# Optimization experiments

Measured on AMD Instinct MI355X. Metric: run time of the kernel, lower is better.

The kernel has to match this reference:

```python
import jax, jax.numpy as jnp
import numpy as np

N_NODES = 100000

def gcn_conv(x, W, b, src, dst, n):
    # PyG GCNConv: h = x @ W; add self-loops; norm = D^-1/2 (A+I) D^-1/2; aggregate at dst.
    h = x @ W  # [N, out]
    deg = jnp.zeros((n,), h.dtype).at[dst].add(1.0) + 1.0  # +1 for self-loop
    d = jax.lax.rsqrt(deg)  # deg >= 1 always
    norm = d[src] * d[dst]  # [E]
    agg = jnp.zeros_like(h).at[dst].add(norm[:, None] * h[src])  # scatter-add neighbor messages
    agg = agg + h * (d * d)[:, None]  # self-loop contribution (norm = d_i^2)
    return agg + b


def setup_inputs() -> dict:
    key = jax.random.key(0)
    k1, k2, k3, k4 = jax.random.split(key, 4)
    F_in, H, C = 128, 64, 16
    E = 3200000
    x = jax.random.normal(k1, (N_NODES, F_in), dtype=jnp.float32)
    edges = jax.random.randint(k2, (E, 2), 0, N_NODES, dtype=jnp.int64)
    # Glorot-style init for weights, zero bias (as in GCNConv.reset_parameters)
    W1 = jax.random.normal(k3, (F_in, H), dtype=jnp.float32) * (1.0 / np.sqrt(F_in))
    b1 = jnp.zeros((H,), jnp.float32)
    W2 = jax.random.normal(k4, (H, C), dtype=jnp.float32) * (1.0 / np.sqrt(H))
    b2 = jnp.zeros((C,), jnp.float32)
    return {"x": x, "edges": edges, "W1": W1, "b1": b1, "W2": W2, "b2": b2}


def reference(x, edges, W1, b1, W2, b2):
    src, dst = edges[:, 0], edges[:, 1]
    h = jax.nn.relu(gcn_conv(x, W1, b1, src, dst, N_NODES))
    out = gcn_conv(h, W2, b2, src, dst, N_NODES)
    return out
```

## Files before the change

kernel.cpp:

```cpp
#include <hip/hip_runtime.h>

#define N_NODES 100000
#define F_IN    128
#define H_DIM   64
#define C_DIM   16
#define NBKT    391
#define CHUNK   8192
#define CAP     8960
#define MAXCH   400

typedef __attribute__((ext_vector_type(8))) short bf16x8;
typedef __attribute__((ext_vector_type(4))) float f32x4;

__device__ __forceinline__ unsigned bfr(float f) {
    unsigned u = __float_as_uint(f);
    return (u + (((u >> 16) & 1u) + 0x7FFFu)) >> 16;
}
__device__ __forceinline__ void accb(float4& a, uint2 u) {
    a.x += __uint_as_float(u.x << 16);
    a.y += __uint_as_float(u.x & 0xFFFF0000u);
    a.z += __uint_as_float(u.y << 16);
    a.w += __uint_as_float(u.y & 0xFFFF0000u);
}

__global__ __launch_bounds__(512) void k_bfill(const int2* __restrict__ edges,
                                               int* __restrict__ pairs_flat,
                                               int* __restrict__ cnts_g,
                                               int* __restrict__ lbase_g, int E) {
    __shared__ int2 sp[CHUNK];
    __shared__ int  cnt[NBKT];
    __shared__ int  lbase[NBKT];
    __shared__ int  scn[512];
    int t = threadIdx.x;
    for (int i = t; i < NBKT; i += 512) cnt[i] = 0;
    __syncthreads();
    int base = blockIdx.x * CHUNK;
    int m    = min(E - base, CHUNK);
    int2 ed[16];
    int  rk[16];
    #pragma unroll
    for (int i = 0; i < 16; ++i) {
        int e = i * 512 + t;
        if (e < m) {
            ed[i] = edges[base + e];
            rk[i] = atomicAdd(&cnt[ed[i].y >> 8], 1);
        }
    }
    __syncthreads();
    scn[t] = (t < NBKT) ? cnt[t] : 0;
    __syncthreads();
    #pragma unroll
    for (int off = 1; off < 512; off <<= 1) {
        int v = (t >= off) ? scn[t - off] : 0;
        __syncthreads();
        scn[t] += v;
        __syncthreads();
    }
    for (int b = t; b < NBKT; b += 512) {
        int c = cnt[b];
        int lb = scn[b] - c;
        lbase[b] = lb;
        cnts_g [blockIdx.x * NBKT + b] = c;
        lbase_g[blockIdx.x * NBKT + b] = lb;
    }
    __syncthreads();
    #pragma unroll
    for (int i = 0; i < 16; ++i) {
        int e = i * 512 + t;
        if (e < m) sp[lbase[ed[i].y >> 8] + rk[i]] = ed[i];
    }
    __syncthreads();
    #pragma unroll
    for (int i = 0; i < 16; ++i) {
        int idx = i * 512 + t;
        if (idx < m) {
            int2 p = sp[idx];
            pairs_flat[base + idx] = (p.x << 8) | (p.y & 255);
        }
    }
}

__global__ __launch_bounds__(1024) void k_bnode(const int* __restrict__ pairs_flat,
                                                const int* __restrict__ cnts_g,
                                                const int* __restrict__ lbase_g,
                                                int* __restrict__ csr_src,
                                                int* __restrict__ node_base,
                                                int* __restrict__ node_cnt,
                                                float* __restrict__ dinv, int nch) {
    __shared__ int spairs[CAP];
    __shared__ int sc[CAP];
    __shared__ int rcnt[MAXCH];
    __shared__ int rlb[MAXCH];
    __shared__ int roff[MAXCH];
    __shared__ int scn[512];
    __shared__ int cnt[256];
    __shared__ int row[256];
    __shared__ int wsum[4];
    __shared__ int mtot;
    int b = blockIdx.x;
    int t = threadIdx.x;
    if (t < 256) cnt[t] = 0;
    for (int i = t; i < nch; i += 1024) {
        rcnt[i] = cnts_g [i * NBKT + b];
        rlb[i]  = lbase_g[i * NBKT + b];
    }
    __syncthreads();
    if (t < 512) scn[t] = (t < nch) ? rcnt[t] : 0;
    __syncthreads();
    #pragma unroll
    for (int off = 1; off < 512; off <<= 1) {
        int v = 0;
        if (t < 512 && t >= off) v = scn[t - off];
        __syncthreads();
        if (t < 512) scn[t] += v;
        __syncthreads();
    }
    if (t < nch) roff[t] = scn[t] - rcnt[t];
    if (t == 0) mtot = scn[nch - 1];
    __syncthreads();
    int m = min(mtot, CAP);
    int grp = t >> 4, l16 = t & 15;
    for (int r = grp; r < nch; r += 64) {
        int c  = rcnt[r];
        int ro = roff[r];
        int rb = r * CHUNK + rlb[r];
        for (int j = l16; j < c; j += 16) {
            int pos = ro + j;
            if (pos < CAP) {
                int p = pairs_flat[rb + j];
                spairs[pos] = p;
                atomicAdd(&cnt[p & 255], 1);
            }
        }
    }
    __syncthreads();
    if (t < 256) {
        int c = cnt[t];
        int lane = t & 63, wv = t >> 6;
        int v = c;
        #pragma unroll
        for (int off = 1; off < 64; off <<= 1) {
            int u = __shfl_up(v, off);
            if (lane >= off) v += u;
        }
        if (lane == 63) wsum[wv] = v;
        __syncthreads();
        int woff = 0;
        #pragma unroll
        for (int w = 0; w < 4; ++w) woff += (w < wv) ? wsum[w] : 0;
        int incl = v + woff;
        row[t] = incl - c;
        int node = b * 256 + t;
        if (node < N_NODES) {
            node_base[node] = b * CAP + incl - c;
            node_cnt[node]  = c;
            dinv[node]      = rsqrtf((float)(c + 1));
        }
    } else {
        __syncthreads();
    }
    __syncthreads();
    for (int e = t; e < m; e += 1024) {
        int p   = spairs[e];
        int pos = atomicAdd(&row[p & 255], 1);
        sc[pos] = ((unsigned)p) >> 8;
    }
    __syncthreads();
    for (int e = t; e < m; e += 1024)
        csr_src[b * CAP + e] = sc[e];
}

__global__ __launch_bounds__(256) void k_gemm1(const float* __restrict__ x,
                                               const float* __restrict__ W1,
                                               const float* __restrict__ dinv,
                                               uint2* __restrict__ g1b) {
    __shared__ short wt[64][132];
    int tid = threadIdx.x;
    {
        int n  = tid & 63;
        int k0 = (tid >> 6) * 32;
        #pragma unroll 8
        for (int k = 0; k < 32; ++k)
            wt[n][k0 + k] = (short)bfr(W1[(size_t)(k0 + k) * H_DIM + n]);
    }
    __syncthreads();

    int wave = tid >> 6, lane = tid & 63;
    int tile = blockIdx.x * 4 + wave;
    bool valid = tile < N_NODES / 16;
    int row0 = (valid ? tile : 0) * 16;
    int l15  = lane & 15;
    int kg   = lane >> 4;
    const float* xrow = x + (size_t)(row0 + l15) * F_IN;

    f32x4 ac0 = {0.f,0.f,0.f,0.f}, ac1 = ac0, ac2 = ac0, ac3 = ac0;
    #pragma unroll
    for (int ks = 0; ks < 4; ++ks) {
        int kb = ks * 32 + kg * 8;
        float4 p0 = *(const float4*)(xrow + kb);
        float4 p1 = *(const float4*)(xrow + kb + 4);
        bf16x8 a;
        a[0] = (short)bfr(p0.x); a[1] = (short)bfr(p0.y);
        a[2] = (short)bfr(p0.z); a[3] = (short)bfr(p0.w);
        a[4] = (short)bfr(p1.x); a[5] = (short)bfr(p1.y);
        a[6] = (short)bfr(p1.z); a[7] = (short)bfr(p1.w);
        bf16x8 b0 = *(const bf16x8*)&wt[l15     ][kb];
        bf16x8 b1 = *(const bf16x8*)&wt[l15 + 16][kb];
        bf16x8 b2 = *(const bf16x8*)&wt[l15 + 32][kb];
        bf16x8 b3 = *(const bf16x8*)&wt[l15 + 48][kb];
        ac0 = __builtin_amdgcn_mfma_f32_16x16x32_bf16(a, b0, ac0, 0, 0, 0);
        ac1 = __builtin_amdgcn_mfma_f32_16x16x32_bf16(a, b1, ac1, 0, 0, 0);
        ac2 = __builtin_amdgcn_mfma_f32_16x16x32_bf16(a, b2, ac2, 0, 0, 0);
        ac3 = __builtin_amdgcn_mfma_f32_16x16x32_bf16(a, b3, ac3, 0, 0, 0);
    }
    if (!valid) return;

    int rbase = row0 + kg * 4;
    #pragma unroll
    for (int r = 0; r < 4; ++r) {
        float di = dinv[rbase + r];
        size_t gro = (size_t)(rbase + r) * 16;
        #pragma unroll
        for (int ct = 0; ct < 4; ++ct) {
            float v = ((ct == 0) ? ac0[r] : (ct == 1) ? ac1[r] :
                       (ct == 2) ? ac2[r] : ac3[r]) * di;
            float v1 = __shfl_down(v, 1);
            float v2 = __shfl_down(v, 2);
            float v3 = __shfl_down(v, 3);
            if ((l15 & 3) == 0) {
                uint2 pk;
                pk.x = bfr(v)  | (bfr(v1) << 16);
                pk.y = bfr(v2) | (bfr(v3) << 16);
                g1b[gro + ct * 4 + (l15 >> 2)] = pk;
            }
        }
    }
}

__global__ __launch_bounds__(256) void k_gather1(const int* __restrict__ csr_src,
                                                 const int* __restrict__ base,
                                                 const int* __restrict__ cnt,
                                                 const float* __restrict__ dinv,
                                                 const uint2* __restrict__ g1b,
                                                 const float* __restrict__ b1,
                                                 const float* __restrict__ W2,
                                                 uint2* __restrict__ g2b) {
    __shared__ float  w2t[16 * 68];
    __shared__ float4 ysh[4][68];
    int tid = threadIdx.x;
    #pragma unroll
    for (int i = 0; i < 4; ++i) {
        int idx = i * 256 + tid;
        w2t[(idx & 15) * 68 + (idx >> 4)] = W2[idx];
    }
    __syncthreads();

    int lane = tid & 63;
    int wv   = tid >> 6;
    int grp  = lane >> 4;
    int l16  = lane & 15;
    int g0   = lane & 48;
    int node = ((blockIdx.x * 256 + tid) >> 6) * 4 + grp;
    int   b  = base[node];
    int   c  = cnt[node];
    float di = dinv[node];
    float4 acc = {0.f, 0.f, 0.f, 0.f};
    accb(acc, g1b[(size_t)node * 16 + l16]);

    for (int k0 = 0; k0 < c; k0 += 16) {
        int k = k0 + l16;
        int sidx = (k < c) ? csr_src[b + k] : 0;
        int nj = min(16, c - k0);
        int j = 0;
        for (; j + 4 <= nj; j += 4) {
            int s0 = __shfl(sidx, g0 + j + 0);
            int s1 = __shfl(sidx, g0 + j + 1);
            int s2 = __shfl(sidx, g0 + j + 2);
            int s3 = __shfl(sidx, g0 + j + 3);
            uint2 u0 = g1b[(size_t)s0 * 16 + l16];
            uint2 u1 = g1b[(size_t)s1 * 16 + l16];
            uint2 u2 = g1b[(size_t)s2 * 16 + l16];
            uint2 u3 = g1b[(size_t)s3 * 16 + l16];
            accb(acc, u0); accb(acc, u1); accb(acc, u2); accb(acc, u3);
        }
        for (; j < nj; ++j) {
            accb(acc, g1b[(size_t)__shfl(sidx, g0 + j) * 16 + l16]);
        }
    }

    float4 bv = ((const float4*)b1)[l16];
    float4 y;
    y.x = fmaxf(fmaf(di, acc.x, bv.x), 0.f) * di;
    y.y = fmaxf(fmaf(di, acc.y, bv.y), 0.f) * di;
    y.z = fmaxf(fmaf(di, acc.z, bv.z), 0.f) * di;
    y.w = fmaxf(fmaf(di, acc.w, bv.w), 0.f) * di;
    ysh[wv][grp * 17 + l16] = y;

    float o = 0.f;
    #pragma unroll
    for (int f4 = 0; f4 < 16; ++f4) {
        float4 yv = ysh[wv][grp * 17 + f4];
        const float4* wr = (const float4*)&w2t[l16 * 68 + f4 * 4];
        float4 wv4 = *wr;
        o = fmaf(yv.x, wv4.x, o);
        o = fmaf(yv.y, wv4.y, o);
        o = fmaf(yv.z, wv4.z, o);
        o = fmaf(yv.w, wv4.w, o);
    }
    float o1 = __shfl_down(o, 1);
    float o2 = __shfl_down(o, 2);
    float o3 = __shfl_down(o, 3);
    if ((l16 & 3) == 0) {
        uint2 pk;
        pk.x = bfr(o)  | (bfr(o1) << 16);
        pk.y = bfr(o2) | (bfr(o3) << 16);
        g2b[(size_t)node * 4 + (l16 >> 2)] = pk;
    }
}

__global__ __launch_bounds__(256) void k_gather2(const int* __restrict__ csr_src,
                                                 const int* __restrict__ base,
                                                 const int* __restrict__ cnt,
                                                 const float* __restrict__ dinv,
                                                 const uint2* __restrict__ g2b,
                                                 const float* __restrict__ b2,
                                                 float* __restrict__ out) {
    int tid  = threadIdx.x;
    int lane = tid & 63;
    int grp  = lane >> 2;
    int l4   = lane & 3;
    int g0   = lane & 60;
    int node = ((blockIdx.x * 256 + tid) >> 6) * 16 + grp;
    if (node >= N_NODES) return;
    int   b  = base[node];
    int   c  = cnt[node];
    float di = dinv[node];
    float4 acc = {0.f, 0.f, 0.f, 0.f};
    accb(acc, g2b[(size_t)node * 4 + l4]);

    for (int k0 = 0; k0 < c; k0 += 4) {
        int k = k0 + l4;
        int sidx = (k < c) ? csr_src[b + k] : 0;
        int nj = min(4, c - k0);
        if (nj == 4) {
            int s0 = __shfl(sidx, g0 + 0);
            int s1 = __shfl(sidx, g0 + 1);
            int s2 = __shfl(sidx, g0 + 2);
            int s3 = __shfl(sidx, g0 + 3);
            uint2 u0 = g2b[(size_t)s0 * 4 + l4];
            uint2 u1 = g2b[(size_t)s1 * 4 + l4];
            uint2 u2 = g2b[(size_t)s2 * 4 + l4];
            uint2 u3 = g2b[(size_t)s3 * 4 + l4];
            accb(acc, u0); accb(acc, u1); accb(acc, u2); accb(acc, u3);
        } else {
            for (int j = 0; j < nj; ++j)
                accb(acc, g2b[(size_t)__shfl(sidx, g0 + j) * 4 + l4]);
        }
    }
    float4 bv = ((const float4*)b2)[l4];
    float4 r  = { fmaf(di, acc.x, bv.x), fmaf(di, acc.y, bv.y),
                  fmaf(di, acc.z, bv.z), fmaf(di, acc.w, bv.w) };
    ((float4*)out)[(size_t)node * 4 + l4] = r;
}

extern "C" void kernel_launch(void* const* d_in, const int* in_sizes, int n_in,
                              void* d_out, int out_size, void* d_ws, size_t ws_size,
                              hipStream_t stream) {
    const float* x     = (const float*)d_in[0];
    const int*   edges = (const int*)d_in[1];
    const float* W1    = (const float*)d_in[2];
    const float* b1    = (const float*)d_in[3];
    const float* W2    = (const float*)d_in[4];
    const float* b2    = (const float*)d_in[5];
    float*       out   = (float*)d_out;

    const int E   = in_sizes[1] / 2;
    const int nch = (E + CHUNK - 1) / CHUNK;

    int*   pairs_flat = (int*)d_ws;
    uint2* g1b     = (uint2*)d_ws;
    uint2* g2b     = (uint2*)((float*)d_ws + (size_t)NBKT * CAP);
    int*   csr_src = (int*)g2b + (size_t)N_NODES * 8 + 64;
    int*   nbase   = csr_src + (size_t)NBKT * CAP;
    int*   ncnt    = nbase + N_NODES;
    float* dinv    = (float*)(ncnt + N_NODES);
    int*   cnts_g  = (int*)(dinv + N_NODES);
    int*   lbase_g = cnts_g + (size_t)nch * NBKT;

    k_bfill <<<nch, 512, 0, stream>>>((const int2*)edges, pairs_flat,
                                      cnts_g, lbase_g, E);
    k_bnode <<<NBKT, 1024, 0, stream>>>(pairs_flat, cnts_g, lbase_g, csr_src,
                                        nbase, ncnt, dinv, nch);

    k_gemm1   <<<(N_NODES / 16 + 3) / 4, 256, 0, stream>>>(x, W1, dinv, g1b);

    k_gather1 <<<6250, 256, 0, stream>>>(csr_src, nbase, ncnt, dinv, g1b, b1, W2, g2b);

    k_gather2 <<<1563, 256, 0, stream>>>(csr_src, nbase, ncnt, dinv, g2b, b2, out);
}
```

Measured before the change: 138.7 us.

## Halve CSR bucket size to 128 nodes and record in-bucket rank during counting

Destination buckets shrink from 256 to 128 nodes, doubling the bucket count so the node-level CSR build runs on twice as many smaller 512-thread blocks with less shared memory each. The in-bucket rank from the counting atomic is packed into the upper bits of each pair, so the second scatter pass needs no atomics. The chunk-offset scan in k_bnode becomes a wave-shuffle scan instead of a barrier-heavy shared-memory scan. In exchange, the fill kernel must scan 1024 entries and write twice as many per-chunk count and offset records. The packing assumes source ids fit in 17 bits and ranks in 8 bits.

```diff
diff --git a/kernel.cpp b/kernel.cpp
--- a/kernel.cpp
+++ b/kernel.cpp
@@ -4,9 +4,9 @@
 #define F_IN    128
 #define H_DIM   64
 #define C_DIM   16
-#define NBKT    391
+#define NBKT2   782
 #define CHUNK   8192
-#define CAP     8960
+#define CAP2    4608
 #define MAXCH   400
 
 typedef __attribute__((ext_vector_type(8))) short bf16x8;
@@ -28,11 +28,11 @@
                                                int* __restrict__ cnts_g,
                                                int* __restrict__ lbase_g, int E) {
     __shared__ int2 sp[CHUNK];
-    __shared__ int  cnt[NBKT];
-    __shared__ int  lbase[NBKT];
-    __shared__ int  scn[512];
+    __shared__ int  cnt[NBKT2];
+    __shared__ int  lbase[NBKT2];
+    __shared__ int  scn[1024];
     int t = threadIdx.x;
-    for (int i = t; i < NBKT; i += 512) cnt[i] = 0;
+    for (int i = t; i < NBKT2; i += 512) cnt[i] = 0;
     __syncthreads();
     int base = blockIdx.x * CHUNK;
     int m    = min(E - base, CHUNK);
@@ -43,31 +43,34 @@
         int e = i * 512 + t;
         if (e < m) {
             ed[i] = edges[base + e];
-            rk[i] = atomicAdd(&cnt[ed[i].y >> 8], 1);
-        }
-    }
-    __syncthreads();
-    scn[t] = (t < NBKT) ? cnt[t] : 0;
-    __syncthreads();
-    #pragma unroll
-    for (int off = 1; off < 512; off <<= 1) {
-        int v = (t >= off) ? scn[t - off] : 0;
-        __syncthreads();
-        scn[t] += v;
-        __syncthreads();
-    }
-    for (int b = t; b < NBKT; b += 512) {
+            rk[i] = atomicAdd(&cnt[ed[i].y >> 7], 1);
+        }
+    }
+    __syncthreads();
+    scn[t]       = (t < NBKT2) ? cnt[t] : 0;
+    scn[t + 512] = (t + 512 < NBKT2) ? cnt[t + 512] : 0;
+    __syncthreads();
+    #pragma unroll
+    for (int off = 1; off < 1024; off <<= 1) {
+        int v0 = (t >= off) ? scn[t - off] : 0;
+        int v1 = (t + 512 >= off) ? scn[t + 512 - off] : 0;
+        __syncthreads();
+        scn[t] += v0;
+        scn[t + 512] += v1;
+        __syncthreads();
+    }
+    for (int b = t; b < NBKT2; b += 512) {
         int c = cnt[b];
         int lb = scn[b] - c;
         lbase[b] = lb;
-        cnts_g [blockIdx.x * NBKT + b] = c;
-        lbase_g[blockIdx.x * NBKT + b] = lb;
+        cnts_g [blockIdx.x * NBKT2 + b] = c;
+        lbase_g[blockIdx.x * NBKT2 + b] = lb;
     }
     __syncthreads();
     #pragma unroll
     for (int i = 0; i < 16; ++i) {
         int e = i * 512 + t;
-        if (e < m) sp[lbase[ed[i].y >> 8] + rk[i]] = ed[i];
+        if (e < m) sp[lbase[ed[i].y >> 7] + rk[i]] = ed[i];
     }
     __syncthreads();
     #pragma unroll
@@ -75,68 +78,71 @@
         int idx = i * 512 + t;
         if (idx < m) {
             int2 p = sp[idx];
-            pairs_flat[base + idx] = (p.x << 8) | (p.y & 255);
-        }
-    }
-}
-
-__global__ __launch_bounds__(1024) void k_bnode(const int* __restrict__ pairs_flat,
-                                                const int* __restrict__ cnts_g,
-                                                const int* __restrict__ lbase_g,
-                                                int* __restrict__ csr_src,
-                                                int* __restrict__ node_base,
-                                                int* __restrict__ node_cnt,
-                                                float* __restrict__ dinv, int nch) {
-    __shared__ int spairs[CAP];
-    __shared__ int sc[CAP];
+            pairs_flat[base + idx] = (p.x << 7) | (p.y & 127);
+        }
+    }
+}
+
+__global__ __launch_bounds__(512) void k_bnode(const int* __restrict__ pairs_flat,
+                                               const int* __restrict__ cnts_g,
+                                               const int* __restrict__ lbase_g,
+                                               int* __restrict__ csr_src,
+                                               int* __restrict__ node_base,
+                                               int* __restrict__ node_cnt,
+                                               float* __restrict__ dinv, int nch) {
+    __shared__ int spairs[CAP2];
+    __shared__ int sc[CAP2];
     __shared__ int rcnt[MAXCH];
     __shared__ int rlb[MAXCH];
     __shared__ int roff[MAXCH];
-    __shared__ int scn[512];
-    __shared__ int cnt[256];
-    __shared__ int row[256];
-    __shared__ int wsum[4];
+    __shared__ int cnt[128];
+    __shared__ int row[128];
+    __shared__ int wsum[8];
     __shared__ int mtot;
     int b = blockIdx.x;
     int t = threadIdx.x;
-    if (t < 256) cnt[t] = 0;
-    for (int i = t; i < nch; i += 1024) {
-        rcnt[i] = cnts_g [i * NBKT + b];
-        rlb[i]  = lbase_g[i * NBKT + b];
-    }
-    __syncthreads();
-    if (t < 512) scn[t] = (t < nch) ? rcnt[t] : 0;
-    __syncthreads();
-    #pragma unroll
-    for (int off = 1; off < 512; off <<= 1) {
-        int v = 0;
-        if (t < 512 && t >= off) v = scn[t - off];
-        __syncthreads();
-        if (t < 512) scn[t] += v;
-        __syncthreads();
-    }
-    if (t < nch) roff[t] = scn[t] - rcnt[t];
-    if (t == 0) mtot = scn[nch - 1];
-    __syncthreads();
-    int m = min(mtot, CAP);
-    int grp = t >> 4, l16 = t & 15;
+    int lane = t & 63, wv = t >> 6;
+    if (t < 128) cnt[t] = 0;
+    for (int i = t; i < nch; i += 512) {
+        rcnt[i] = cnts_g [i * NBKT2 + b];
+        rlb[i]  = lbase_g[i * NBKT2 + b];
+    }
+    __syncthreads();
+    {
+        int v = (t < nch) ? rcnt[t] : 0;
+        int s = v;
+        #pragma unroll
+        for (int off = 1; off < 64; off <<= 1) {
+            int u = __shfl_up(s, off);
+            if (lane >= off) s += u;
+        }
+        if (lane == 63) wsum[wv] = s;
+        __syncthreads();
+        int woff = 0;
+        #pragma unroll
+        for (int w = 0; w < 8; ++w) woff += (w < wv) ? wsum[w] : 0;
+        if (t < nch) roff[t] = s + woff - v;
+        if (t == nch - 1) mtot = s + woff;
+        __syncthreads();
+    }
+    int m = min(mtot, CAP2);
+    int grp = t >> 3, l8 = t & 7;
     for (int r = grp; r < nch; r += 64) {
         int c  = rcnt[r];
         int ro = roff[r];
         int rb = r * CHUNK + rlb[r];
-        for (int j = l16; j < c; j += 16) {
+        for (int j = l8; j < c; j += 8) {
             int pos = ro + j;
-            if (pos < CAP) {
-                int p = pairs_flat[rb + j];
-                spairs[pos] = p;
-                atomicAdd(&cnt[p & 255], 1);
+            if (pos < CAP2) {
+                int p  = pairs_flat[rb + j];
+                int rk = atomicAdd(&cnt[p & 127], 1);
+                spairs[pos] = p | (rk << 24);
             }
         }
     }
     __syncthreads();
-    if (t < 256) {
+    if (t < 128) {
         int c = cnt[t];
-        int lane = t & 63, wv = t >> 6;
         int v = c;
         #pragma unroll
         for (int off = 1; off < 64; off <<= 1) {
@@ -145,14 +151,11 @@
         }
         if (lane == 63) wsum[wv] = v;
         __syncthreads();
-        int woff = 0;
-        #pragma unroll
-        for (int w = 0; w < 4; ++w) woff += (w < wv) ? wsum[w] : 0;
-        int incl = v + woff;
+        int incl = v + ((wv == 1) ? wsum[0] : 0);
         row[t] = incl - c;
-        int node = b * 256 + t;
+        int node = b * 128 + t;
         if (node < N_NODES) {
-            node_base[node] = b * CAP + incl - c;
+            node_base[node] = b * CAP2 + incl - c;
             node_cnt[node]  = c;
             dinv[node]      = rsqrtf((float)(c + 1));
         }
@@ -160,14 +163,13 @@
         __syncthreads();
     }
     __syncthreads();
-    for (int e = t; e < m; e += 1024) {
-        int p   = spairs[e];
-        int pos = atomicAdd(&row[p & 255], 1);
-        sc[pos] = ((unsigned)p) >> 8;
-    }
-    __syncthreads();
-    for (int e = t; e < m; e += 1024)
-        csr_src[b * CAP + e] = sc[e];
+    for (int e = t; e < m; e += 512) {
+        int p = spairs[e];
+        sc[row[p & 127] + ((unsigned)p >> 24)] = (p >> 7) & 0x1FFFF;
+    }
+    __syncthreads();
+    for (int e = t; e < m; e += 512)
+        csr_src[b * CAP2 + e] = sc[e];
 }
 
 __global__ __launch_bounds__(256) void k_gemm1(const float* __restrict__ x,
@@ -379,17 +381,17 @@
 
     int*   pairs_flat = (int*)d_ws;
     uint2* g1b     = (uint2*)d_ws;
-    uint2* g2b     = (uint2*)((float*)d_ws + (size_t)NBKT * CAP);
+    uint2* g2b     = (uint2*)((float*)d_ws + 3600000);
     int*   csr_src = (int*)g2b + (size_t)N_NODES * 8 + 64;
-    int*   nbase   = csr_src + (size_t)NBKT * CAP;
+    int*   nbase   = csr_src + (size_t)NBKT2 * CAP2;
     int*   ncnt    = nbase + N_NODES;
     float* dinv    = (float*)(ncnt + N_NODES);
     int*   cnts_g  = (int*)(dinv + N_NODES);
-    int*   lbase_g = cnts_g + (size_t)nch * NBKT;
+    int*   lbase_g = cnts_g + (size_t)nch * NBKT2;
 
     k_bfill <<<nch, 512, 0, stream>>>((const int2*)edges, pairs_flat,
                                       cnts_g, lbase_g, E);
-    k_bnode <<<NBKT, 1024, 0, stream>>>(pairs_flat, cnts_g, lbase_g, csr_src,
+    k_bnode <<<NBKT2, 512, 0, stream>>>(pairs_flat, cnts_g, lbase_g, csr_src,
                                         nbase, ncnt, dinv, nch);
 
     k_gemm1   <<<(N_NODES / 16 + 3) / 4, 256, 0, stream>>>(x, W1, dinv, g1b);
```

Result: slower. 146.9 us (+5.9%).
